# Optimization experiments

Hardware: AMD Instinct MI355X
Metric: run time of the kernel (lower is better)

Reference implementation:

```python
import jax, jax.numpy as jnp
import numpy as np

B, A, G, C = 64, 8732, 50, 81
NEG_POS_RATIO = 3


def _make_boxes(key, b, n):
    k1, k2 = jax.random.split(key)
    mins = jax.random.uniform(k1, (b, n, 2)) * 0.7
    sizes = jax.random.uniform(k2, (b, n, 2)) * 0.3 + 0.01
    return jnp.concatenate([mins, mins + sizes], axis=-1)  # [b,n,4] xyxy


def setup_inputs() -> dict:
    key = jax.random.key(0)
    k1, k2, k3, k4 = jax.random.split(key, 4)
    pred_boxes = _make_boxes(k1, B, A)
    gt_boxes = _make_boxes(k2, B, G)
    pred_scores = jax.random.normal(k3, (B, A, C), dtype=jnp.float32)
    gt_labels = jax.random.randint(k4, (B, G), 0, C)
    return {"pred_boxes": pred_boxes, "pred_scores": pred_scores,
            "gt_boxes": gt_boxes, "gt_labels": gt_labels}


def _iou(a, b):
    # a: [B,A,4], b: [B,G,4] -> [B,A,G]
    a_ = a[:, :, None, :]
    b_ = b[:, None, :, :]
    iw = jnp.clip(jnp.minimum(a_[..., 2], b_[..., 2]) - jnp.maximum(a_[..., 0], b_[..., 0]), 0)
    ih = jnp.clip(jnp.minimum(a_[..., 3], b_[..., 3]) - jnp.maximum(a_[..., 1], b_[..., 1]), 0)
    inter = iw * ih
    area_a = (a_[..., 2] - a_[..., 0]) * (a_[..., 3] - a_[..., 1])
    area_b = (b_[..., 2] - b_[..., 0]) * (b_[..., 3] - b_[..., 1])
    union = jnp.clip(area_a + area_b - inter, 1e-6)
    return inter / union


def reference(pred_boxes, pred_scores, gt_boxes, gt_labels):
    num_anchors = pred_boxes.shape[1]
    iou = _iou(pred_boxes, gt_boxes)              # [B,A,G]
    best_iou = iou.max(axis=2)                    # [B,A]
    best_idx = iou.argmax(axis=2)                 # [B,A]
    pos = best_iou > 0.5

    matched_boxes = jnp.take_along_axis(gt_boxes, best_idx[..., None], axis=1)   # [B,A,4]
    matched_labels = jnp.take_along_axis(gt_labels, best_idx, axis=1)            # [B,A]
    target_boxes = jnp.where(pos[..., None], matched_boxes, 0.0)
    target_labels = jnp.where(pos, matched_labels, 0)

    pos_mask = target_labels > 0
    num_pos = pos_mask.sum(axis=1)                # [B]

    # smooth L1 (beta=1), summed over box coords
    d = pred_boxes - target_boxes
    ad = jnp.abs(d)
    sl1 = jnp.where(ad < 1.0, 0.5 * d * d, ad - 0.5).sum(axis=2)  # [B,A]
    loc_loss = (sl1 * pos_mask).sum()

    # cross entropy per anchor
    log_p = jax.nn.log_softmax(pred_scores, axis=-1)
    conf = -jnp.take_along_axis(log_p, target_labels[..., None], axis=-1)[..., 0]  # [B,A]

    conf_pos = (conf * pos_mask).sum()

    # hard negative mining: top (3*num_pos) losses among negatives
    conf_neg = jnp.where(pos_mask, -1.0, conf)
    num_neg = jnp.minimum(NEG_POS_RATIO * num_pos, num_anchors - 1)   # [B]
    order = jnp.argsort(-conf_neg, axis=1)        # descending
    rank = jnp.argsort(order, axis=1)             # rank of each anchor in sorted order
    hard_neg = rank < num_neg[:, None]
    conf_neg_hard = (conf * hard_neg).sum()

    total = (loc_loss + conf_pos + conf_neg_hard) / jnp.maximum(num_pos, 1).sum()
    return total
```

## Files before the change

kernel.cpp:

```cpp
#include <hip/hip_runtime.h>
#include <hip/hip_bf16.h>

#define BB 64
#define AA 8732
#define GG 50
#define CC 81
#define NEG_RATIO 3
#define HW 16
#define HSTRIDE 257
#define NCHUNK 137
#define XB 16


__device__ __forceinline__ unsigned mono_key(float f) {
    unsigned u = __float_as_uint(f);
    u = (u & 0x80000000u) ? ~u : (u | 0x80000000u);
    return ~u;
}

__global__ __launch_bounds__(256, 4) void k_match(
    const float* __restrict__ pred_boxes, const float* __restrict__ pred_scores,
    const float* __restrict__ gt_boxes, const int* __restrict__ gt_labels,
    float* __restrict__ conf_out, float* __restrict__ confneg_out,
    float* __restrict__ acc_slots, int* __restrict__ np_slots)
{
    __shared__ float4 sgt[GG];
    __shared__ float  sarea[GG];
    __shared__ int    slab[GG];
    __shared__ float  redf[4];
    __shared__ int    redi[4];

    const int tid = threadIdx.x;
    const int b = blockIdx.y;
    const int x = blockIdx.x;
    const int grp = tid >> 2;
    const int q   = tid & 3;

    if (tid < GG) {
        const float* gp = gt_boxes + ((size_t)b * GG + tid) * 4;
        float4 g4 = make_float4(gp[0], gp[1], gp[2], gp[3]);
        sgt[tid] = g4;
        sarea[tid] = (g4.z - g4.x) * (g4.w - g4.y);
        slab[tid] = gt_labels[b * GG + tid];
    }
    __syncthreads();

    const float*  sb = pred_scores + (size_t)b * AA * CC;
    const float4* bbx = (const float4*)pred_boxes + (size_t)b * AA;

    float contrib = 0.f;
    int npos = 0;

    int a0 = x * 64 + grp;
    int am = a0 < AA ? a0 : AA - 1;
    float4 nbox = bbx[am];
    const float* nrow = sb + (size_t)am * CC;
    float4 ns0 = *(const float4*)(nrow + 4 * q);
    float4 ns1 = *(const float4*)(nrow + 4 * q + 16);
    float4 ns2 = *(const float4*)(nrow + 4 * q + 32);
    float4 ns3 = *(const float4*)(nrow + 4 * q + 48);
    float4 ns4 = *(const float4*)(nrow + 4 * q + 64);
    float  ns80 = nrow[80];

    for (int c = x; c < NCHUNK; c += XB) {
        const float4 pb = nbox;
        const float4 s0 = ns0, s1 = ns1, s2 = ns2, s3 = ns3, s4 = ns4;
        const float  s80 = ns80;
        const int a = c * 64 + grp;
        const bool valid = a < AA;

        int cn = c + XB; if (cn >= NCHUNK) cn = c;
        int an = cn * 64 + grp; if (an >= AA) an = AA - 1;
        nbox = bbx[an];
        const float* prow = sb + (size_t)an * CC;
        ns0 = *(const float4*)(prow + 4 * q);
        ns1 = *(const float4*)(prow + 4 * q + 16);
        ns2 = *(const float4*)(prow + 4 * q + 32);
        ns3 = *(const float4*)(prow + 4 * q + 48);
        ns4 = *(const float4*)(prow + 4 * q + 64);
        ns80 = prow[80];

        const float area_p = (pb.z - pb.x) * (pb.w - pb.y);
        float best = -1.f; int bidx = 0x7fffffff;
        for (int g = q; g < GG; g += 4) {
            float4 gb = sgt[g];
            float iw = fmaxf(fminf(pb.z, gb.z) - fmaxf(pb.x, gb.x), 0.f);
            float ih = fmaxf(fminf(pb.w, gb.w) - fmaxf(pb.y, gb.y), 0.f);
            float inter = iw * ih;
            float uni = fmaxf(area_p + sarea[g] - inter, 1e-6f);
            float iou = __fdividef(inter, uni);
            if (iou > best) { best = iou; bidx = g; }
        }
        #pragma unroll
        for (int off = 1; off < 4; off <<= 1) {
            float ov = __shfl_xor(best, off);
            int   oi = __shfl_xor(bidx, off);
            if (ov > best || (ov == best && oi < bidx)) { best = ov; bidx = oi; }
        }
        const int label = (best > 0.5f) ? slab[bidx] : 0;

        float sm = 0.f, labv = 0.f;
        {
            const float4 vv[5] = {s0, s1, s2, s3, s4};
            #pragma unroll
            for (int t = 0; t < 5; ++t) {
                const float4 v = vv[t];
                sm += __expf(v.x) + __expf(v.y) + __expf(v.z) + __expf(v.w);
                const int f = q + (t << 2);
                if ((label >> 2) == f) {
                    const int r = label & 3;
                    labv = (r == 0) ? v.x : (r == 1) ? v.y : (r == 2) ? v.z : v.w;
                }
            }
            if (q == 0) {
                sm += __expf(s80);
                if (label == 80) labv = s80;
            }
        }
        sm   += __shfl_xor(sm, 1);   sm   += __shfl_xor(sm, 2);
        labv += __shfl_xor(labv, 1); labv += __shfl_xor(labv, 2);
        const float conf = __logf(sm) - labv;

        if (q == 0 && valid) {
            const size_t ai = (size_t)b * AA + a;
            conf_out[ai] = conf;
            const bool pm = label > 0;
            confneg_out[ai] = pm ? -1.f : conf;
            if (pm) {
                npos++;
                const float4 gb = sgt[bidx];
                float sl1 = 0.f, d, ad;
                d = pb.x - gb.x; ad = fabsf(d); sl1 += (ad < 1.f) ? 0.5f * d * d : ad - 0.5f;
                d = pb.y - gb.y; ad = fabsf(d); sl1 += (ad < 1.f) ? 0.5f * d * d : ad - 0.5f;
                d = pb.z - gb.z; ad = fabsf(d); sl1 += (ad < 1.f) ? 0.5f * d * d : ad - 0.5f;
                d = pb.w - gb.w; ad = fabsf(d); sl1 += (ad < 1.f) ? 0.5f * d * d : ad - 0.5f;
                contrib += sl1 + conf;
            }
        }
    }

    #pragma unroll
    for (int off = 32; off; off >>= 1) {
        contrib += __shfl_down(contrib, off);
        npos    += __shfl_down(npos, off);
    }
    const int wv = tid >> 6;
    if ((tid & 63) == 0) { redf[wv] = contrib; redi[wv] = npos; }
    __syncthreads();
    if (tid == 0) {
        acc_slots[b * XB + x] = redf[0] + redf[1] + redf[2] + redf[3];
        np_slots[b * XB + x]  = redi[0] + redi[1] + redi[2] + redi[3];
    }
}

__global__ __launch_bounds__(1024) void k_hardneg(
    const float* __restrict__ confneg, const float* __restrict__ conf,
    const int* __restrict__ np_slots, float* __restrict__ hn_slots)
{
    __shared__ unsigned hist[HW * HSTRIDE];
    __shared__ unsigned binsum[256];
    __shared__ unsigned sel[2];
    __shared__ unsigned uE[HW], uG[HW], eb[HW];
    __shared__ float    fred[HW];
    __shared__ int      stot;

    const int b = blockIdx.x;
    const int tid = threadIdx.x;
    const int wv = tid >> 6;
    const int lane = tid & 63;

    int np = 0;
    #pragma unroll
    for (int i = 0; i < XB; ++i) np += np_slots[b * XB + i];
    int k = NEG_RATIO * np; if (k > AA - 1) k = AA - 1;
    if (k <= 0) {
        if (tid == 0) hn_slots[b] = 0.f;
        return;
    }

    const float* cn  = confneg + (size_t)b * AA;
    const float* cfp = conf    + (size_t)b * AA;

    const int lo = tid * 9;
    int nk = AA - lo; nk = nk > 9 ? 9 : (nk < 0 ? 0 : nk);
    unsigned keys[9]; float vals[9];
    #pragma unroll
    for (int j = 0; j < 9; ++j) {
        if (j < nk) { keys[j] = mono_key(cn[lo + j]); vals[j] = cfp[lo + j]; }
    }

    unsigned prefix = 0, kk = (unsigned)k;
    for (int lev = 0; lev < 4; ++lev) {
        const int shift = 24 - 8 * lev;
        for (int i = tid; i < HW * HSTRIDE; i += 1024) hist[i] = 0;
        __syncthreads();
        #pragma unroll
        for (int j = 0; j < 9; ++j) {
            if (j < nk) {
                const unsigned key = keys[j];
                if (lev == 0 || (key >> (shift + 8)) == prefix)
                    atomicAdd(&hist[wv * HSTRIDE + ((key >> shift) & 255u)], 1u);
            }
        }
        __syncthreads();
        if (tid < 256) {
            unsigned s = 0;
            #pragma unroll
            for (int w = 0; w < HW; ++w) s += hist[w * HSTRIDE + tid];
            binsum[tid] = s;
        }
        __syncthreads();
        if (wv == 0) {
            const unsigned v0 = binsum[4 * lane], v1 = binsum[4 * lane + 1];
            const unsigned v2 = binsum[4 * lane + 2], v3 = binsum[4 * lane + 3];
            const unsigned lsum = v0 + v1 + v2 + v3;
            unsigned sc = lsum;
            #pragma unroll
            for (int off = 1; off < 64; off <<= 1) {
                unsigned t = __shfl_up(sc, off);
                if (lane >= off) sc += t;
            }
            const unsigned excl = sc - lsum;
            if (kk > excl && kk <= sc) {
                unsigned cacc = excl;
                if (kk <= cacc + v0)              { sel[0] = 4 * lane;     sel[1] = kk - cacc; }
                else if (kk <= (cacc += v0) + v1) { sel[0] = 4 * lane + 1; sel[1] = kk - cacc; }
                else if (kk <= (cacc += v1) + v2) { sel[0] = 4 * lane + 2; sel[1] = kk - cacc; }
                else                              { sel[0] = 4 * lane + 3; sel[1] = kk - cacc - v2; }
            }
        }
        __syncthreads();
        prefix = (prefix << 8) | sel[0];
        kk = sel[1];
    }
    const unsigned kth = prefix;

    int cntG = 0, cntE = 0; float sum_gt = 0.f;
    #pragma unroll
    for (int j = 0; j < 9; ++j) {
        if (j < nk) {
            if (keys[j] < kth)       { cntG++; sum_gt += vals[j]; }
            else if (keys[j] == kth) { cntE++; }
        }
    }
    int sc = cntE;
    #pragma unroll
    for (int off = 1; off < 64; off <<= 1) {
        int t = __shfl_up(sc, off);
        if (lane >= off) sc += t;
    }
    int gt = cntG;
    #pragma unroll
    for (int off = 32; off; off >>= 1) gt += __shfl_down(gt, off);
    if (lane == 63) uE[wv] = (unsigned)sc;
    if (lane == 0)  uG[wv] = (unsigned)gt;
    __syncthreads();
    if (wv == 0) {
        unsigned e = (lane < HW) ? uE[lane] : 0u;
        unsigned g = (lane < HW) ? uG[lane] : 0u;
        unsigned se = e;
        #pragma unroll
        for (int off = 1; off < 16; off <<= 1) {
            unsigned t = __shfl_up(se, off);
            if (lane >= off) se += t;
        }
        if (lane < HW) eb[lane] = se - e;
        #pragma unroll
        for (int off = 8; off; off >>= 1) g += __shfl_down(g, off);
        if (lane == 0) stot = (int)g;
    }
    __syncthreads();
    const int m = k - stot;
    const int exclE = (int)eb[wv] + (sc - cntE);

    float sum_eq = 0.f;
    if (m > 0 && cntE > 0) {
        int seen = 0;
        #pragma unroll
        for (int j = 0; j < 9; ++j) {
            if (j < nk && keys[j] == kth) {
                if (exclE + seen < m) sum_eq += vals[j];
                seen++;
            }
        }
    }

    float contrib = sum_gt + sum_eq;
    #pragma unroll
    for (int off = 32; off; off >>= 1) contrib += __shfl_down(contrib, off);
    if (lane == 0) fred[wv] = contrib;
    __syncthreads();
    if (tid == 0) {
        float t = 0.f;
        #pragma unroll
        for (int w = 0; w < HW; ++w) t += fred[w];
        hn_slots[b] = t;
    }
}

__global__ __launch_bounds__(256) void k_final(
    const float* __restrict__ acc_slots, const int* __restrict__ np_slots,
    const float* __restrict__ hn_slots, float* __restrict__ out)
{
    __shared__ float sf[4];
    __shared__ int   si[4];
    const int tid = threadIdx.x;
    const int lane = tid & 63, wv = tid >> 6;

    float v = acc_slots[4 * tid] + acc_slots[4 * tid + 1]
            + acc_slots[4 * tid + 2] + acc_slots[4 * tid + 3];
    int den = 0;
    if (tid < BB) {
        v += hn_slots[tid];
        int np = 0;
        #pragma unroll
        for (int i = 0; i < XB; ++i) np += np_slots[tid * XB + i];
        den = np > 1 ? np : 1;
    }
    #pragma unroll
    for (int off = 32; off; off >>= 1) {
        v   += __shfl_down(v, off);
        den += __shfl_down(den, off);
    }
    if (lane == 0) { sf[wv] = v; si[wv] = den; }
    __syncthreads();
    if (tid == 0)
        out[0] = (sf[0] + sf[1] + sf[2] + sf[3]) / (float)(si[0] + si[1] + si[2] + si[3]);
}

extern "C" void kernel_launch(void* const* d_in, const int* in_sizes, int n_in,
                              void* d_out, int out_size, void* d_ws, size_t ws_size,
                              hipStream_t stream) {
    const float* pred_boxes  = (const float*)d_in[0];
    const float* pred_scores = (const float*)d_in[1];
    const float* gt_boxes    = (const float*)d_in[2];
    const int*   gt_labels   = (const int*)d_in[3];

    float* ws        = (float*)d_ws;
    float* acc_slots = ws;
    int*   np_slots  = (int*)(ws + 1024);
    float* hn_slots  = ws + 2048;
    float* conf      = ws + 4096;
    float* conf_neg  = conf + (size_t)BB * AA;


    dim3 g1(XB, BB);
    k_match<<<g1, 256, 0, stream>>>(pred_boxes, pred_scores, gt_boxes, gt_labels,
                                    conf, conf_neg, acc_slots, np_slots);
    k_hardneg<<<BB, 1024, 0, stream>>>(conf_neg, conf, np_slots, hn_slots);
    k_final<<<1, 256, 0, stream>>>(acc_slots, np_slots, hn_slots, (float*)d_out);
}
```

Measured before the change: 293.0 us.

## Drop conf buffer, fuse final reduction into hard-negative kernel via last-block counter

Stops writing the separate conf array and recovers negative loss values in the hard-negative kernel by inverting the monotone sort key of conf_neg. The final reduction kernel is removed: each hard-negative block publishes its per-batch sums, and the last block to arrive (tracked with an atomic counter reset in k_match) computes the output. The label logit is now read directly from the score row instead of being selected through shuffles, and the IoU loop is unrolled with a fixed trip count. This saves one global write/read stream and one kernel launch, at the cost of atomic/fence ordering subtleties.

```diff
diff --git a/kernel.cpp b/kernel.cpp
--- a/kernel.cpp
+++ b/kernel.cpp
@@ -1,5 +1,4 @@
 #include <hip/hip_runtime.h>
-#include <hip/hip_bf16.h>
 
 #define BB 64
 #define AA 8732
@@ -18,11 +17,17 @@
     return ~u;
 }
 
+__device__ __forceinline__ float unkey_val(unsigned key) {
+    unsigned u = ~key;
+    return __uint_as_float((u & 0x80000000u) ? (u & 0x7fffffffu) : ~u);
+}
+
 __global__ __launch_bounds__(256, 4) void k_match(
     const float* __restrict__ pred_boxes, const float* __restrict__ pred_scores,
     const float* __restrict__ gt_boxes, const int* __restrict__ gt_labels,
-    float* __restrict__ conf_out, float* __restrict__ confneg_out,
-    float* __restrict__ acc_slots, int* __restrict__ np_slots)
+    float* __restrict__ confneg_out,
+    float* __restrict__ acc_slots, int* __restrict__ np_slots,
+    unsigned* __restrict__ ctr)
 {
     __shared__ float4 sgt[GG];
     __shared__ float  sarea[GG];
@@ -36,9 +41,10 @@
     const int grp = tid >> 2;
     const int q   = tid & 3;
 
+    if (b == 0 && x == 0 && tid == 0) *ctr = 0u;
+
     if (tid < GG) {
-        const float* gp = gt_boxes + ((size_t)b * GG + tid) * 4;
-        float4 g4 = make_float4(gp[0], gp[1], gp[2], gp[3]);
+        float4 g4 = ((const float4*)gt_boxes)[b * GG + tid];
         sgt[tid] = g4;
         sarea[tid] = (g4.z - g4.x) * (g4.w - g4.y);
         slab[tid] = gt_labels[b * GG + tid];
@@ -66,30 +72,36 @@
         const float4 pb = nbox;
         const float4 s0 = ns0, s1 = ns1, s2 = ns2, s3 = ns3, s4 = ns4;
         const float  s80 = ns80;
+        const float* crow = nrow;
         const int a = c * 64 + grp;
         const bool valid = a < AA;
 
-        int cn = c + XB; if (cn >= NCHUNK) cn = c;
-        int an = cn * 64 + grp; if (an >= AA) an = AA - 1;
+        int cnx = c + XB; if (cnx >= NCHUNK) cnx = c;
+        int an = cnx * 64 + grp; if (an >= AA) an = AA - 1;
         nbox = bbx[an];
-        const float* prow = sb + (size_t)an * CC;
-        ns0 = *(const float4*)(prow + 4 * q);
-        ns1 = *(const float4*)(prow + 4 * q + 16);
-        ns2 = *(const float4*)(prow + 4 * q + 32);
-        ns3 = *(const float4*)(prow + 4 * q + 48);
-        ns4 = *(const float4*)(prow + 4 * q + 64);
-        ns80 = prow[80];
+        nrow = sb + (size_t)an * CC;
+        ns0 = *(const float4*)(nrow + 4 * q);
+        ns1 = *(const float4*)(nrow + 4 * q + 16);
+        ns2 = *(const float4*)(nrow + 4 * q + 32);
+        ns3 = *(const float4*)(nrow + 4 * q + 48);
+        ns4 = *(const float4*)(nrow + 4 * q + 64);
+        ns80 = nrow[80];
 
         const float area_p = (pb.z - pb.x) * (pb.w - pb.y);
         float best = -1.f; int bidx = 0x7fffffff;
-        for (int g = q; g < GG; g += 4) {
-            float4 gb = sgt[g];
+        #pragma unroll
+        for (int i = 0; i < 13; ++i) {
+            const int g = q + (i << 2);
+            const bool gv = g < GG;
+            const int gc = gv ? g : 0;
+            const float4 gb = sgt[gc];
+            const float  sa = sarea[gc];
             float iw = fmaxf(fminf(pb.z, gb.z) - fmaxf(pb.x, gb.x), 0.f);
             float ih = fmaxf(fminf(pb.w, gb.w) - fmaxf(pb.y, gb.y), 0.f);
             float inter = iw * ih;
-            float uni = fmaxf(area_p + sarea[g] - inter, 1e-6f);
+            float uni = fmaxf(area_p + sa - inter, 1e-6f);
             float iou = __fdividef(inter, uni);
-            if (iou > best) { best = iou; bidx = g; }
+            if (gv && iou > best) { best = iou; bidx = g; }
         }
         #pragma unroll
         for (int off = 1; off < 4; off <<= 1) {
@@ -99,31 +111,20 @@
         }
         const int label = (best > 0.5f) ? slab[bidx] : 0;
 
-        float sm = 0.f, labv = 0.f;
-        {
-            const float4 vv[5] = {s0, s1, s2, s3, s4};
-            #pragma unroll
-            for (int t = 0; t < 5; ++t) {
-                const float4 v = vv[t];
-                sm += __expf(v.x) + __expf(v.y) + __expf(v.z) + __expf(v.w);
-                const int f = q + (t << 2);
-                if ((label >> 2) == f) {
-                    const int r = label & 3;
-                    labv = (r == 0) ? v.x : (r == 1) ? v.y : (r == 2) ? v.z : v.w;
-                }
-            }
-            if (q == 0) {
-                sm += __expf(s80);
-                if (label == 80) labv = s80;
-            }
-        }
-        sm   += __shfl_xor(sm, 1);   sm   += __shfl_xor(sm, 2);
-        labv += __shfl_xor(labv, 1); labv += __shfl_xor(labv, 2);
-        const float conf = __logf(sm) - labv;
+        float sm = 0.f;
+        sm += __expf(s0.x) + __expf(s0.y) + __expf(s0.z) + __expf(s0.w);
+        sm += __expf(s1.x) + __expf(s1.y) + __expf(s1.z) + __expf(s1.w);
+        sm += __expf(s2.x) + __expf(s2.y) + __expf(s2.z) + __expf(s2.w);
+        sm += __expf(s3.x) + __expf(s3.y) + __expf(s3.z) + __expf(s3.w);
+        sm += __expf(s4.x) + __expf(s4.y) + __expf(s4.z) + __expf(s4.w);
+        if (q == 0) sm += __expf(s80);
+        sm += __shfl_xor(sm, 1);
+        sm += __shfl_xor(sm, 2);
 
         if (q == 0 && valid) {
+            const float labv = crow[label];
+            const float conf = __logf(sm) - labv;
             const size_t ai = (size_t)b * AA + a;
-            conf_out[ai] = conf;
             const bool pm = label > 0;
             confneg_out[ai] = pm ? -1.f : conf;
             if (pm) {
@@ -154,8 +155,10 @@
 }
 
 __global__ __launch_bounds__(1024) void k_hardneg(
-    const float* __restrict__ confneg, const float* __restrict__ conf,
-    const int* __restrict__ np_slots, float* __restrict__ hn_slots)
+    const float* __restrict__ confneg,
+    const int* __restrict__ np_slots, const float* __restrict__ acc_slots,
+    float* __restrict__ per_b, int* __restrict__ den_b,
+    unsigned* __restrict__ ctr, float* __restrict__ out)
 {
     __shared__ unsigned hist[HW * HSTRIDE];
     __shared__ unsigned binsum[256];
@@ -163,6 +166,7 @@
     __shared__ unsigned uE[HW], uG[HW], eb[HW];
     __shared__ float    fred[HW];
     __shared__ int      stot;
+    __shared__ int      slast;
 
     const int b = blockIdx.x;
     const int tid = threadIdx.x;
@@ -173,159 +177,146 @@
     #pragma unroll
     for (int i = 0; i < XB; ++i) np += np_slots[b * XB + i];
     int k = NEG_RATIO * np; if (k > AA - 1) k = AA - 1;
-    if (k <= 0) {
-        if (tid == 0) hn_slots[b] = 0.f;
-        return;
-    }
-
-    const float* cn  = confneg + (size_t)b * AA;
-    const float* cfp = conf    + (size_t)b * AA;
-
-    const int lo = tid * 9;
-    int nk = AA - lo; nk = nk > 9 ? 9 : (nk < 0 ? 0 : nk);
-    unsigned keys[9]; float vals[9];
-    #pragma unroll
-    for (int j = 0; j < 9; ++j) {
-        if (j < nk) { keys[j] = mono_key(cn[lo + j]); vals[j] = cfp[lo + j]; }
-    }
-
-    unsigned prefix = 0, kk = (unsigned)k;
-    for (int lev = 0; lev < 4; ++lev) {
-        const int shift = 24 - 8 * lev;
-        for (int i = tid; i < HW * HSTRIDE; i += 1024) hist[i] = 0;
-        __syncthreads();
+
+    float hn = 0.f;
+    if (k > 0) {
+        const float* cn = confneg + (size_t)b * AA;
+
+        const int lo = tid * 9;
+        int nk = AA - lo; nk = nk > 9 ? 9 : (nk < 0 ? 0 : nk);
+        unsigned keys[9];
+        #pragma unroll
+        for (int j = 0; j < 9; ++j)
+            if (j < nk) keys[j] = mono_key(cn[lo + j]);
+
+        unsigned prefix = 0, kk = (unsigned)k;
+        for (int lev = 0; lev < 4; ++lev) {
+            const int shift = 24 - 8 * lev;
+            for (int i = tid; i < HW * HSTRIDE; i += 1024) hist[i] = 0;
+            __syncthreads();
+            #pragma unroll
+            for (int j = 0; j < 9; ++j) {
+                if (j < nk) {
+                    const unsigned key = keys[j];
+                    if (lev == 0 || (key >> (shift + 8)) == prefix)
+                        atomicAdd(&hist[wv * HSTRIDE + ((key >> shift) & 255u)], 1u);
+                }
+            }
+            __syncthreads();
+            if (tid < 256) {
+                unsigned s = 0;
+                #pragma unroll
+                for (int w = 0; w < HW; ++w) s += hist[w * HSTRIDE + tid];
+                binsum[tid] = s;
+            }
+            __syncthreads();
+            if (wv == 0) {
+                const unsigned v0 = binsum[4 * lane], v1 = binsum[4 * lane + 1];
+                const unsigned v2 = binsum[4 * lane + 2], v3 = binsum[4 * lane + 3];
+                const unsigned lsum = v0 + v1 + v2 + v3;
+                unsigned sc = lsum;
+                #pragma unroll
+                for (int off = 1; off < 64; off <<= 1) {
+                    unsigned t = __shfl_up(sc, off);
+                    if (lane >= off) sc += t;
+                }
+                const unsigned excl = sc - lsum;
+                if (kk > excl && kk <= sc) {
+                    unsigned cacc = excl;
+                    if (kk <= cacc + v0)              { sel[0] = 4 * lane;     sel[1] = kk - cacc; }
+                    else if (kk <= (cacc += v0) + v1) { sel[0] = 4 * lane + 1; sel[1] = kk - cacc; }
+                    else if (kk <= (cacc += v1) + v2) { sel[0] = 4 * lane + 2; sel[1] = kk - cacc; }
+                    else                              { sel[0] = 4 * lane + 3; sel[1] = kk - cacc - v2; }
+                }
+            }
+            __syncthreads();
+            prefix = (prefix << 8) | sel[0];
+            kk = sel[1];
+        }
+        const unsigned kth = prefix;
+
+        int cntG = 0, cntE = 0; float sum_gt = 0.f;
         #pragma unroll
         for (int j = 0; j < 9; ++j) {
             if (j < nk) {
-                const unsigned key = keys[j];
-                if (lev == 0 || (key >> (shift + 8)) == prefix)
-                    atomicAdd(&hist[wv * HSTRIDE + ((key >> shift) & 255u)], 1u);
-            }
-        }
-        __syncthreads();
-        if (tid < 256) {
-            unsigned s = 0;
-            #pragma unroll
-            for (int w = 0; w < HW; ++w) s += hist[w * HSTRIDE + tid];
-            binsum[tid] = s;
-        }
+                if (keys[j] < kth)       { cntG++; sum_gt += unkey_val(keys[j]); }
+                else if (keys[j] == kth) { cntE++; }
+            }
+        }
+        int sc = cntE;
+        #pragma unroll
+        for (int off = 1; off < 64; off <<= 1) {
+            int t = __shfl_up(sc, off);
+            if (lane >= off) sc += t;
+        }
+        int gt = cntG;
+        #pragma unroll
+        for (int off = 32; off; off >>= 1) gt += __shfl_down(gt, off);
+        if (lane == 63) uE[wv] = (unsigned)sc;
+        if (lane == 0)  uG[wv] = (unsigned)gt;
         __syncthreads();
         if (wv == 0) {
-            const unsigned v0 = binsum[4 * lane], v1 = binsum[4 * lane + 1];
-            const unsigned v2 = binsum[4 * lane + 2], v3 = binsum[4 * lane + 3];
-            const unsigned lsum = v0 + v1 + v2 + v3;
-            unsigned sc = lsum;
-            #pragma unroll
-            for (int off = 1; off < 64; off <<= 1) {
-                unsigned t = __shfl_up(sc, off);
-                if (lane >= off) sc += t;
-            }
-            const unsigned excl = sc - lsum;
-            if (kk > excl && kk <= sc) {
-                unsigned cacc = excl;
-                if (kk <= cacc + v0)              { sel[0] = 4 * lane;     sel[1] = kk - cacc; }
-                else if (kk <= (cacc += v0) + v1) { sel[0] = 4 * lane + 1; sel[1] = kk - cacc; }
-                else if (kk <= (cacc += v1) + v2) { sel[0] = 4 * lane + 2; sel[1] = kk - cacc; }
-                else                              { sel[0] = 4 * lane + 3; sel[1] = kk - cacc - v2; }
-            }
+            unsigned e = (lane < HW) ? uE[lane] : 0u;
+            unsigned g = (lane < HW) ? uG[lane] : 0u;
+            unsigned se = e;
+            #pragma unroll
+            for (int off = 1; off < 16; off <<= 1) {
+                unsigned t = __shfl_up(se, off);
+                if (lane >= off) se += t;
+            }
+            if (lane < HW) eb[lane] = se - e;
+            #pragma unroll
+            for (int off = 8; off; off >>= 1) g += __shfl_down(g, off);
+            if (lane == 0) stot = (int)g;
         }
         __syncthreads();
-        prefix = (prefix << 8) | sel[0];
-        kk = sel[1];
-    }
-    const unsigned kth = prefix;
-
-    int cntG = 0, cntE = 0; float sum_gt = 0.f;
-    #pragma unroll
-    for (int j = 0; j < 9; ++j) {
-        if (j < nk) {
-            if (keys[j] < kth)       { cntG++; sum_gt += vals[j]; }
-            else if (keys[j] == kth) { cntE++; }
-        }
-    }
-    int sc = cntE;
-    #pragma unroll
-    for (int off = 1; off < 64; off <<= 1) {
-        int t = __shfl_up(sc, off);
-        if (lane >= off) sc += t;
-    }
-    int gt = cntG;
-    #pragma unroll
-    for (int off = 32; off; off >>= 1) gt += __shfl_down(gt, off);
-    if (lane == 63) uE[wv] = (unsigned)sc;
-    if (lane == 0)  uG[wv] = (unsigned)gt;
+        const int m = k - stot;
+        const int exclE = (int)eb[wv] + (sc - cntE);
+
+        float sum_eq = 0.f;
+        if (m > 0 && cntE > 0) {
+            int seen = 0;
+            #pragma unroll
+            for (int j = 0; j < 9; ++j) {
+                if (j < nk && keys[j] == kth) {
+                    if (exclE + seen < m) sum_eq += unkey_val(keys[j]);
+                    seen++;
+                }
+            }
+        }
+
+        float contrib = sum_gt + sum_eq;
+        #pragma unroll
+        for (int off = 32; off; off >>= 1) contrib += __shfl_down(contrib, off);
+        if (lane == 0) fred[wv] = contrib;
+        __syncthreads();
+        if (tid == 0) {
+            #pragma unroll
+            for (int w = 0; w < HW; ++w) hn += fred[w];
+        }
+    }
+
+    if (tid == 0) {
+        float accb = 0.f;
+        #pragma unroll
+        for (int i = 0; i < XB; ++i) accb += acc_slots[b * XB + i];
+        atomicExch(&per_b[b], accb + hn);
+        atomicExch(&den_b[b], np > 1 ? np : 1);
+        __threadfence();
+        unsigned prev = atomicAdd(ctr, 1u);
+        slast = (prev == (unsigned)(BB - 1)) ? 1 : 0;
+    }
     __syncthreads();
-    if (wv == 0) {
-        unsigned e = (lane < HW) ? uE[lane] : 0u;
-        unsigned g = (lane < HW) ? uG[lane] : 0u;
-        unsigned se = e;
-        #pragma unroll
-        for (int off = 1; off < 16; off <<= 1) {
-            unsigned t = __shfl_up(se, off);
-            if (lane >= off) se += t;
-        }
-        if (lane < HW) eb[lane] = se - e;
-        #pragma unroll
-        for (int off = 8; off; off >>= 1) g += __shfl_down(g, off);
-        if (lane == 0) stot = (int)g;
-    }
-    __syncthreads();
-    const int m = k - stot;
-    const int exclE = (int)eb[wv] + (sc - cntE);
-
-    float sum_eq = 0.f;
-    if (m > 0 && cntE > 0) {
-        int seen = 0;
-        #pragma unroll
-        for (int j = 0; j < 9; ++j) {
-            if (j < nk && keys[j] == kth) {
-                if (exclE + seen < m) sum_eq += vals[j];
-                seen++;
-            }
-        }
-    }
-
-    float contrib = sum_gt + sum_eq;
-    #pragma unroll
-    for (int off = 32; off; off >>= 1) contrib += __shfl_down(contrib, off);
-    if (lane == 0) fred[wv] = contrib;
-    __syncthreads();
-    if (tid == 0) {
-        float t = 0.f;
-        #pragma unroll
-        for (int w = 0; w < HW; ++w) t += fred[w];
-        hn_slots[b] = t;
-    }
-}
-
-__global__ __launch_bounds__(256) void k_final(
-    const float* __restrict__ acc_slots, const int* __restrict__ np_slots,
-    const float* __restrict__ hn_slots, float* __restrict__ out)
-{
-    __shared__ float sf[4];
-    __shared__ int   si[4];
-    const int tid = threadIdx.x;
-    const int lane = tid & 63, wv = tid >> 6;
-
-    float v = acc_slots[4 * tid] + acc_slots[4 * tid + 1]
-            + acc_slots[4 * tid + 2] + acc_slots[4 * tid + 3];
-    int den = 0;
-    if (tid < BB) {
-        v += hn_slots[tid];
-        int np = 0;
-        #pragma unroll
-        for (int i = 0; i < XB; ++i) np += np_slots[tid * XB + i];
-        den = np > 1 ? np : 1;
-    }
-    #pragma unroll
-    for (int off = 32; off; off >>= 1) {
-        v   += __shfl_down(v, off);
-        den += __shfl_down(den, off);
-    }
-    if (lane == 0) { sf[wv] = v; si[wv] = den; }
-    __syncthreads();
-    if (tid == 0)
-        out[0] = (sf[0] + sf[1] + sf[2] + sf[3]) / (float)(si[0] + si[1] + si[2] + si[3]);
+    if (slast && tid < BB) {
+        float v = atomicAdd(&per_b[tid], 0.f);
+        int   d = atomicAdd(&den_b[tid], 0);
+        #pragma unroll
+        for (int off = 32; off; off >>= 1) {
+            v += __shfl_down(v, off);
+            d += __shfl_down(d, off);
+        }
+        if (tid == 0) out[0] = v / (float)d;
+    }
 }
 
 extern "C" void kernel_launch(void* const* d_in, const int* in_sizes, int n_in,
@@ -336,17 +327,17 @@
     const float* gt_boxes    = (const float*)d_in[2];
     const int*   gt_labels   = (const int*)d_in[3];
 
-    float* ws        = (float*)d_ws;
-    float* acc_slots = ws;
-    int*   np_slots  = (int*)(ws + 1024);
-    float* hn_slots  = ws + 2048;
-    float* conf      = ws + 4096;
-    float* conf_neg  = conf + (size_t)BB * AA;
-
+    float*    ws        = (float*)d_ws;
+    float*    acc_slots = ws;
+    int*      np_slots  = (int*)(ws + 1024);
+    float*    per_b     = ws + 2048;
+    int*      den_b     = (int*)(ws + 2112);
+    unsigned* ctr       = (unsigned*)(ws + 2176);
+    float*    conf_neg  = ws + 4096;
 
     dim3 g1(XB, BB);
     k_match<<<g1, 256, 0, stream>>>(pred_boxes, pred_scores, gt_boxes, gt_labels,
-                                    conf, conf_neg, acc_slots, np_slots);
-    k_hardneg<<<BB, 1024, 0, stream>>>(conf_neg, conf, np_slots, hn_slots);
-    k_final<<<1, 256, 0, stream>>>(acc_slots, np_slots, hn_slots, (float*)d_out);
-}
+                                    conf_neg, acc_slots, np_slots, ctr);
+    k_hardneg<<<BB, 1024, 0, stream>>>(conf_neg, np_slots, acc_slots,
+                                       per_b, den_b, ctr, (float*)d_out);
+}
```

Measured after the change: 300.7 us (median of 4 runs). 1.03x slower.
